# Kernel tuning notes

Hardware: AMD Instinct MI355X
Metric: run time of the kernel (lower is better)

Reference implementation:

```python
import jax, jax.numpy as jnp
import numpy as np

N = 50000
E = 800000
IN_C = 128
HID = 64
HEADS = 4
NEG_SLOPE = 0.2
EPS = 1e-16


def setup_inputs() -> dict:
    key = jax.random.key(0)
    ks = jax.random.split(key, 12)
    x = jax.random.normal(ks[0], (N, IN_C), dtype=jnp.float32)
    edge_index = jax.random.randint(ks[1], (2, E), 0, N, dtype=jnp.int64)
    # layer 1: in -> (HEADS, HID), concat heads
    W1 = jax.random.normal(ks[2], (IN_C, HEADS * HID), dtype=jnp.float32) * (1.0 / np.sqrt(IN_C))
    a_src1 = jax.random.normal(ks[3], (HEADS, HID), dtype=jnp.float32) * 0.1
    a_dst1 = jax.random.normal(ks[4], (HEADS, HID), dtype=jnp.float32) * 0.1
    b1 = jnp.zeros((HEADS * HID,), dtype=jnp.float32)
    # layer 2: HEADS*HID -> (1, HID)
    W2 = jax.random.normal(ks[5], (HEADS * HID, HID), dtype=jnp.float32) * (1.0 / np.sqrt(HEADS * HID))
    a_src2 = jax.random.normal(ks[6], (1, HID), dtype=jnp.float32) * 0.1
    a_dst2 = jax.random.normal(ks[7], (1, HID), dtype=jnp.float32) * 0.1
    b2 = jnp.zeros((HID,), dtype=jnp.float32)
    return {"x": x, "edge_index": edge_index, "W1": W1, "a_src1": a_src1,
            "a_dst1": a_dst1, "b1": b1, "W2": W2, "a_src2": a_src2,
            "a_dst2": a_dst2, "b2": b2}


def _gat_conv(x, src, dst, W, a_src, a_dst, bias, heads, ch):
    n = x.shape[0]
    h = (x @ W).reshape(n, heads, ch)                       # [N,H,C]
    alpha_s = jnp.einsum('nhc,hc->nh', h, a_src)            # [N,H]
    alpha_d = jnp.einsum('nhc,hc->nh', h, a_dst)            # [N,H]
    e = jax.nn.leaky_relu(alpha_s[src] + alpha_d[dst], NEG_SLOPE)  # [E,H]
    # segment softmax over incoming edges of each dst node
    m = jax.ops.segment_max(e, dst, num_segments=n)         # [N,H]
    ex = jnp.exp(e - m[dst])
    denom = jax.ops.segment_sum(ex, dst, num_segments=n)    # [N,H]
    alpha = ex / (denom[dst] + EPS)                         # [E,H]
    msg = h[src] * alpha[:, :, None]                        # [E,H,C]
    out = jax.ops.segment_sum(msg, dst, num_segments=n)     # [N,H,C]
    return out.reshape(n, heads * ch) + bias


def reference(x, edge_index, W1, a_src1, a_dst1, b1, W2, a_src2, a_dst2, b2):
    src = edge_index[0]
    dst = edge_index[1]
    h = _gat_conv(x, src, dst, W1, a_src1, a_dst1, b1, HEADS, HID)
    h = jax.nn.elu(h)
    h = _gat_conv(h, src, dst, W2, a_src2, a_dst2, b2, 1, HID)
    h = jax.nn.elu(h)
    return h  # [N, HID] (output_dim == hidden_channels so no final linear)
```

## Files before the change

### kernel.cpp

```cpp
#include <hip/hip_runtime.h>
#include <math.h>

#define NN 50000
#define EE 800000
#define IN_C 128
#define HID 64
#define HEADS 4
#define EEP 950000
#define SCAN_BLOCKS ((NN + 255) / 256)
#define EBLOCKS ((EE + 255) / 256)

typedef __attribute__((ext_vector_type(8))) short bf16x8;
typedef __attribute__((ext_vector_type(4))) float f32x4;

#if defined(__has_builtin)
#if __has_builtin(__builtin_amdgcn_fdot2_f32_bf16)
#define HAVE_FDOT2_BF16 1
#endif
#endif


__device__ inline unsigned short f2bf(float f) {
    unsigned u = __float_as_uint(f);
    return (unsigned short)((u + 0x7fff + ((u >> 16) & 1)) >> 16);
}
__device__ inline float bf2f(unsigned short s) {
    return __uint_as_float(((unsigned)s) << 16);
}
__device__ inline unsigned prm(unsigned a, unsigned b, unsigned sel) {
    return __builtin_amdgcn_perm(a, b, sel);
}
#ifdef HAVE_FDOT2_BF16
typedef __attribute__((ext_vector_type(2))) __bf16 bf2v;
__device__ inline float fdot2bf(unsigned h, unsigned w, float acc) {
    return __builtin_amdgcn_fdot2_f32_bf16(__builtin_bit_cast(bf2v, h),
                                           __builtin_bit_cast(bf2v, w), acc, false);
}
#else
__device__ inline float fdot2bf(unsigned h, unsigned w, float acc) {
    return acc + bf2f((unsigned short)(h & 0xffff)) * bf2f((unsigned short)(w & 0xffff))
               + bf2f((unsigned short)(h >> 16)) * bf2f((unsigned short)(w >> 16));
}
#endif

__device__ inline int wave_incl_scan(int v, int lane) {
    #pragma unroll
    for (int off = 1; off < 64; off <<= 1) {
        int t = __shfl_up(v, off);
        if (lane >= off) v += t;
    }
    return v;
}

__device__ inline int block256_excl_scan(int v, int tid, int* ws4) {
    int lane = tid & 63, wv = tid >> 6;
    int incl = wave_incl_scan(v, lane);
    if (lane == 63) ws4[wv] = incl;
    __syncthreads();
    if (tid == 0) {
        int run = 0;
        #pragma unroll
        for (int i = 0; i < 4; i++) { int t = ws4[i]; ws4[i] = run; run += t; }
    }
    __syncthreads();
    return incl + ws4[wv] - v;
}


__global__ void front_kernel(const int* __restrict__ ei, int* __restrict__ deg,
                             unsigned short* __restrict__ rank,
                             const float* __restrict__ W1, unsigned short* __restrict__ W1Thi,
                             unsigned short* __restrict__ W1Tlo,
                             const float* __restrict__ W2, unsigned short* __restrict__ W2Thi,
                             unsigned short* __restrict__ W2Tlo) {
    int b = blockIdx.x;
    int tid = threadIdx.x;
    if (b < EBLOCKS) {
        int i = b * 256 + tid;
        if (i < EE) rank[i] = (unsigned short)atomicAdd(&deg[ei[EE + i]], 1);
    } else if (b < EBLOCKS + 128) {
        int idx = (b - EBLOCKS) * 256 + tid;
        int r = idx >> 8, c = idx & 255;
        float v = W1[idx];
        unsigned short h = f2bf(v);
        W1Thi[c * 128 + r] = h;
        W1Tlo[c * 128 + r] = f2bf(v - bf2f(h));
    } else {
        int idx = (b - EBLOCKS - 128) * 256 + tid;
        int r = idx >> 6, c = idx & 63;
        float v = W2[idx];
        unsigned short h = f2bf(v);
        W2Thi[c * 256 + r] = h;
        W2Tlo[c * 256 + r] = f2bf(v - bf2f(h));
    }
}

__global__ void scan_fill_kernel(const int* __restrict__ deg,
                                 unsigned long long* __restrict__ desc,
                                 int* __restrict__ row_ptr,
                                 unsigned short* __restrict__ csr_src) {
    __shared__ int ws4[4];
    __shared__ int sbase;
    int b = blockIdx.x, tid = threadIdx.x;
    int idx = b * 256 + tid;
    int draw = (idx < NN) ? deg[idx] : 0;
    int d = (draw + 3) & ~3;
    int excl = block256_excl_scan(d, tid, ws4);
    if (tid == 255) {
        unsigned total = (unsigned)(excl + d);
        __threadfence();
        atomicExch(&desc[b], (1ULL << 32) | (unsigned long long)total);
    }
    if (tid < 64) {
        int sum = 0;
        int hi = b;
        while (hi > 0) {
            int lo = hi - 64; if (lo < 0) lo = 0;
            int myi = lo + tid;
            unsigned v = 0;
            if (myi < hi) {
                unsigned long long d8;
                do { d8 = atomicAdd(&desc[myi], 0ULL); } while ((d8 >> 32) == 0);
                v = (unsigned)(d8 & 0xffffffffULL);
            }
            #pragma unroll
            for (int off = 32; off; off >>= 1) v += __shfl_down(v, off);
            v = __shfl(v, 0);
            sum += (int)v;
            hi = lo;
        }
        if (tid == 0) sbase = sum;
    }
    __syncthreads();
    int gbase = sbase;
    if (idx < NN) {
        int rp = gbase + excl;
        row_ptr[idx] = rp;
        for (int p = rp + draw; p < rp + d; ++p) csr_src[p] = 0;
    }
    if (b == gridDim.x - 1 && tid == 255) row_ptr[NN] = gbase + excl + d;
}

__global__ void scatter_kernel(const int* __restrict__ ei, const unsigned short* __restrict__ rank,
                               const int* __restrict__ row_ptr, unsigned short* __restrict__ csr_src) {
    int i = blockIdx.x * blockDim.x + threadIdx.x;
    if (i < EE) {
        int d = ei[EE + i];
        csr_src[row_ptr[d] + (int)rank[i]] = (unsigned short)ei[i];
    }
}

__global__ __launch_bounds__(256) void gemm1_mfma(
        const float* __restrict__ x,
        const unsigned short* __restrict__ Bhi, const unsigned short* __restrict__ Blo,
        const float* __restrict__ a_src, const float* __restrict__ a_dst,
        unsigned short* __restrict__ h1b, float* __restrict__ as1, float* __restrict__ ad1) {
    __shared__ unsigned short Ahi[64][136];
    __shared__ unsigned short Alo[64][136];
    int tid = threadIdx.x;
    int w = tid >> 6, lane = tid & 63;
    int lq = lane >> 4, lr = lane & 15;
    int brow = blockIdx.x * 64;
    {
        int row = tid >> 2;
        int col0 = (tid & 3) * 32;
        int gr = min(brow + row, NN - 1);
        #pragma unroll
        for (int i = 0; i < 32; i += 4) {
            float4 v = *(const float4*)(x + (size_t)gr * 128 + col0 + i);
            unsigned short h0 = f2bf(v.x), h1 = f2bf(v.y), h2 = f2bf(v.z), h3 = f2bf(v.w);
            Ahi[row][col0 + i + 0] = h0; Alo[row][col0 + i + 0] = f2bf(v.x - bf2f(h0));
            Ahi[row][col0 + i + 1] = h1; Alo[row][col0 + i + 1] = f2bf(v.y - bf2f(h1));
            Ahi[row][col0 + i + 2] = h2; Alo[row][col0 + i + 2] = f2bf(v.z - bf2f(h2));
            Ahi[row][col0 + i + 3] = h3; Alo[row][col0 + i + 3] = f2bf(v.w - bf2f(h3));
        }
    }
    __syncthreads();
    f32x4 acc[4][4];
    f32x4 zf = {0.f, 0.f, 0.f, 0.f};
    #pragma unroll
    for (int mi = 0; mi < 4; mi++)
        #pragma unroll
        for (int ni = 0; ni < 4; ni++) acc[mi][ni] = zf;
    #pragma unroll
    for (int q = 0; q < 4; q++) {
        int ko = q * 32 + lq * 8;
        bf16x8 ah[4], al[4];
        #pragma unroll
        for (int mi = 0; mi < 4; mi++) {
            ah[mi] = *(const bf16x8*)(const void*)&Ahi[mi * 16 + lr][ko];
            al[mi] = *(const bf16x8*)(const void*)&Alo[mi * 16 + lr][ko];
        }
        #pragma unroll
        for (int ni = 0; ni < 4; ni++) {
            size_t bo = (size_t)(w * 64 + ni * 16 + lr) * 128 + ko;
            bf16x8 bh = *(const bf16x8*)(const void*)(Bhi + bo);
            bf16x8 bl = *(const bf16x8*)(const void*)(Blo + bo);
            #pragma unroll
            for (int mi = 0; mi < 4; mi++) {
                acc[mi][ni] = __builtin_amdgcn_mfma_f32_16x16x32_bf16(al[mi], bh, acc[mi][ni], 0, 0, 0);
                acc[mi][ni] = __builtin_amdgcn_mfma_f32_16x16x32_bf16(ah[mi], bl, acc[mi][ni], 0, 0, 0);
                acc[mi][ni] = __builtin_amdgcn_mfma_f32_16x16x32_bf16(ah[mi], bh, acc[mi][ni], 0, 0, 0);
            }
        }
    }
    float asv[4], adv[4];
    #pragma unroll
    for (int ni = 0; ni < 4; ni++) {
        asv[ni] = a_src[w * 64 + ni * 16 + lr];
        adv[ni] = a_dst[w * 64 + ni * 16 + lr];
    }
    #pragma unroll
    for (int mi = 0; mi < 4; mi++) {
        f32x4 ps = zf, pd = zf;
        #pragma unroll
        for (int ni = 0; ni < 4; ni++)
            #pragma unroll
            for (int r = 0; r < 4; r++) {
                ps[r] += acc[mi][ni][r] * asv[ni];
                pd[r] += acc[mi][ni][r] * adv[ni];
            }
        #pragma unroll
        for (int m = 1; m < 16; m <<= 1)
            #pragma unroll
            for (int r = 0; r < 4; r++) {
                ps[r] += __shfl_xor(ps[r], m);
                pd[r] += __shfl_xor(pd[r], m);
            }
        #pragma unroll
        for (int r = 0; r < 4; r++) {
            int n = brow + mi * 16 + lq * 4 + r;
            if (lr == 0 && n < NN) { as1[n * 4 + w] = ps[r]; ad1[n * 4 + w] = pd[r]; }
        }
        #pragma unroll
        for (int ni = 0; ni < 4; ni++)
            #pragma unroll
            for (int r = 0; r < 4; r++) {
                int n = brow + mi * 16 + lq * 4 + r;
                if (n < NN)
                    h1b[(size_t)n * 256 + w * 64 + ni * 16 + lr] = f2bf(acc[mi][ni][r]);
            }
    }
}

__global__ __launch_bounds__(256) void gemm2_mfma(
        const unsigned short* __restrict__ Ab,
        const unsigned short* __restrict__ Bhi, const unsigned short* __restrict__ Blo,
        const float* __restrict__ a_src, const float* __restrict__ a_dst,
        unsigned short* __restrict__ g2b, float* __restrict__ as2, float* __restrict__ ad2) {
    int tid = threadIdx.x;
    int w = tid >> 6, lane = tid & 63;
    int lq = lane >> 4, lr = lane & 15;
    int wrow = blockIdx.x * 128 + w * 32;
    f32x4 acc[2][4];
    f32x4 zf = {0.f, 0.f, 0.f, 0.f};
    #pragma unroll
    for (int mi = 0; mi < 2; mi++)
        #pragma unroll
        for (int ni = 0; ni < 4; ni++) acc[mi][ni] = zf;
    int ra = min(wrow + lr, NN - 1);
    int rb = min(wrow + 16 + lr, NN - 1);
    #pragma unroll
    for (int q = 0; q < 8; q++) {
        int ko = q * 32 + lq * 8;
        bf16x8 ah0 = *(const bf16x8*)(const void*)(Ab + (size_t)ra * 256 + ko);
        bf16x8 ah1 = *(const bf16x8*)(const void*)(Ab + (size_t)rb * 256 + ko);
        #pragma unroll
        for (int ni = 0; ni < 4; ni++) {
            size_t bo = (size_t)(ni * 16 + lr) * 256 + ko;
            bf16x8 bh = *(const bf16x8*)(const void*)(Bhi + bo);
            bf16x8 bl = *(const bf16x8*)(const void*)(Blo + bo);
            acc[0][ni] = __builtin_amdgcn_mfma_f32_16x16x32_bf16(ah0, bl, acc[0][ni], 0, 0, 0);
            acc[0][ni] = __builtin_amdgcn_mfma_f32_16x16x32_bf16(ah0, bh, acc[0][ni], 0, 0, 0);
            acc[1][ni] = __builtin_amdgcn_mfma_f32_16x16x32_bf16(ah1, bl, acc[1][ni], 0, 0, 0);
            acc[1][ni] = __builtin_amdgcn_mfma_f32_16x16x32_bf16(ah1, bh, acc[1][ni], 0, 0, 0);
        }
    }
    float asv[4], adv[4];
    #pragma unroll
    for (int ni = 0; ni < 4; ni++) {
        asv[ni] = a_src[ni * 16 + lr];
        adv[ni] = a_dst[ni * 16 + lr];
    }
    #pragma unroll
    for (int mi = 0; mi < 2; mi++) {
        f32x4 ps = zf, pd = zf;
        #pragma unroll
        for (int ni = 0; ni < 4; ni++)
            #pragma unroll
            for (int r = 0; r < 4; r++) {
                ps[r] += acc[mi][ni][r] * asv[ni];
                pd[r] += acc[mi][ni][r] * adv[ni];
            }
        #pragma unroll
        for (int m = 1; m < 16; m <<= 1)
            #pragma unroll
            for (int r = 0; r < 4; r++) {
                ps[r] += __shfl_xor(ps[r], m);
                pd[r] += __shfl_xor(pd[r], m);
            }
        #pragma unroll
        for (int r = 0; r < 4; r++) {
            int n = wrow + mi * 16 + lq * 4 + r;
            if (lr == 0 && n < NN) { as2[n] = ps[r]; ad2[n] = pd[r]; }
        }
        #pragma unroll
        for (int ni = 0; ni < 4; ni++)
            #pragma unroll
            for (int r = 0; r < 4; r++) {
                int n = wrow + mi * 16 + lq * 4 + r;
                if (n < NN)
                    g2b[(size_t)n * 64 + ni * 16 + lr] = f2bf(acc[mi][ni][r]);
            }
    }
}

__global__ __launch_bounds__(256, 4) void agg1_kernel(
        const unsigned short* __restrict__ h1b, const int* __restrict__ row_ptr,
        const int* __restrict__ deg, const unsigned short* __restrict__ csr_src,
        const float* __restrict__ as, const float* __restrict__ ad,
        const float* __restrict__ b1, unsigned short* __restrict__ h2b) {
    __shared__ unsigned ssrc32[4][32];
    __shared__ unsigned wpk[4][4][33];
    int tid = threadIdx.x;
    int wv = tid >> 6, lane = tid & 63;
    int n = blockIdx.x * 4 + wv;
    if (n >= NN) return;
    int start = row_ptr[n], end = row_ptr[n + 1];
    int real_end = start + deg[n];
    int H = lane >> 5, l5 = lane & 31;
    int h = l5 >> 3;
    const unsigned short* __restrict__ hp = h1b + l5 * 8;
    float4 adv = ((const float4*)ad)[n];
    f32x4 a0 = {0.f, 0.f, 0.f, 0.f}, a1 = {0.f, 0.f, 0.f, 0.f};
    float d0 = 0.f, d1 = 0.f, d2 = 0.f, d3 = 0.f;
    uint4 LA0, LB0, LA1, LB1;
    unsigned wp0, wp1;
    for (int c0 = start; c0 < end; c0 += 64) {
        int m = min(64, end - c0);
        if (lane < (m >> 1))
            ssrc32[wv][lane] = *(const unsigned*)(const void*)(csr_src + c0 + 2 * lane);
        float x0 = 0.f, x1 = 0.f, x2 = 0.f, x3 = 0.f;
        if (c0 + lane < real_end) {
            int s = (int)csr_src[c0 + lane];
            float4 av = ((const float4*)as)[s];
            float e0 = av.x + adv.x; e0 = e0 > 0.f ? e0 : 0.2f * e0; x0 = __expf(e0);
            float e1 = av.y + adv.y; e1 = e1 > 0.f ? e1 : 0.2f * e1; x1 = __expf(e1);
            float e2 = av.z + adv.z; e2 = e2 > 0.f ? e2 : 0.2f * e2; x2 = __expf(e2);
            float e3 = av.w + adv.w; e3 = e3 > 0.f ? e3 : 0.2f * e3; x3 = __expf(e3);
            d0 += x0; d1 += x1; d2 += x2; d3 += x3;
        }
        unsigned p0 = f2bf(x0), p1 = f2bf(x1), p2 = f2bf(x2), p3 = f2bf(x3);
        unsigned q0 = (unsigned)__shfl_down((int)p0, 1);
        unsigned q1 = (unsigned)__shfl_down((int)p1, 1);
        unsigned q2 = (unsigned)__shfl_down((int)p2, 1);
        unsigned q3 = (unsigned)__shfl_down((int)p3, 1);
        if (((lane & 1) == 0) && lane < m) {
            wpk[wv][0][lane >> 1] = p0 | (q0 << 16);
            wpk[wv][1][lane >> 1] = p1 | (q1 << 16);
            wpk[wv][2][lane >> 1] = p2 | (q2 << 16);
            wpk[wv][3][lane >> 1] = p3 | (q3 << 16);
        }
        int G = m >> 2;
        auto LD = [&](int g, uint4& A, uint4& B, unsigned& wp) {
            unsigned both = ssrc32[wv][2 * g + H];
            int ia = (int)(both & 0xffffu), ib = (int)(both >> 16);
            A = *(const uint4*)(const void*)(hp + ia * 256);
            B = *(const uint4*)(const void*)(hp + ib * 256);
            wp = wpk[wv][h][2 * g + H];
        };
        auto CMP = [&](const uint4& A, const uint4& B, unsigned wp) {
            a0.x = fdot2bf(prm(B.x, A.x, 0x05040100), wp, a0.x);
            a0.y = fdot2bf(prm(B.x, A.x, 0x07060302), wp, a0.y);
            a0.z = fdot2bf(prm(B.y, A.y, 0x05040100), wp, a0.z);
            a0.w = fdot2bf(prm(B.y, A.y, 0x07060302), wp, a0.w);
            a1.x = fdot2bf(prm(B.z, A.z, 0x05040100), wp, a1.x);
            a1.y = fdot2bf(prm(B.z, A.z, 0x07060302), wp, a1.y);
            a1.z = fdot2bf(prm(B.w, A.w, 0x05040100), wp, a1.z);
            a1.w = fdot2bf(prm(B.w, A.w, 0x07060302), wp, a1.w);
        };
        LD(0, LA0, LB0, wp0);
        if (G > 1) LD(1, LA1, LB1, wp1);
        int g = 0;
        while (true) {
            CMP(LA0, LB0, wp0);
            if (g + 2 < G) LD(g + 2, LA0, LB0, wp0);
            if (++g >= G) break;
            CMP(LA1, LB1, wp1);
            if (g + 2 < G) LD(g + 2, LA1, LB1, wp1);
            if (++g >= G) break;
        }
    }
    #pragma unroll
    for (int off = 32; off; off >>= 1) {
        d0 += __shfl_down(d0, off); d1 += __shfl_down(d1, off);
        d2 += __shfl_down(d2, off); d3 += __shfl_down(d3, off);
    }
    d0 = __shfl(d0, 0); d1 = __shfl(d1, 0);
    d2 = __shfl(d2, 0); d3 = __shfl(d3, 0);
    float den = h == 0 ? d0 : h == 1 ? d1 : h == 2 ? d2 : d3;
    a0.x += __shfl_xor(a0.x, 32); a0.y += __shfl_xor(a0.y, 32);
    a0.z += __shfl_xor(a0.z, 32); a0.w += __shfl_xor(a0.w, 32);
    a1.x += __shfl_xor(a1.x, 32); a1.y += __shfl_xor(a1.y, 32);
    a1.z += __shfl_xor(a1.z, 32); a1.w += __shfl_xor(a1.w, 32);
    if (H == 0) {
        float inv = 1.f / (den + 1e-16f);
        float4 bb0 = *(const float4*)(b1 + l5 * 8);
        float4 bb1 = *(const float4*)(b1 + l5 * 8 + 4);
        float r0 = a0.x * inv + bb0.x, r1 = a0.y * inv + bb0.y;
        float r2 = a0.z * inv + bb0.z, r3 = a0.w * inv + bb0.w;
        float r4 = a1.x * inv + bb1.x, r5 = a1.y * inv + bb1.y;
        float r6 = a1.z * inv + bb1.z, r7 = a1.w * inv + bb1.w;
        r0 = r0 > 0.f ? r0 : expm1f(r0); r1 = r1 > 0.f ? r1 : expm1f(r1);
        r2 = r2 > 0.f ? r2 : expm1f(r2); r3 = r3 > 0.f ? r3 : expm1f(r3);
        r4 = r4 > 0.f ? r4 : expm1f(r4); r5 = r5 > 0.f ? r5 : expm1f(r5);
        r6 = r6 > 0.f ? r6 : expm1f(r6); r7 = r7 > 0.f ? r7 : expm1f(r7);
        uint4 st;
        st.x = (unsigned)f2bf(r0) | ((unsigned)f2bf(r1) << 16);
        st.y = (unsigned)f2bf(r2) | ((unsigned)f2bf(r3) << 16);
        st.z = (unsigned)f2bf(r4) | ((unsigned)f2bf(r5) << 16);
        st.w = (unsigned)f2bf(r6) | ((unsigned)f2bf(r7) << 16);
        *(uint4*)(void*)(h2b + (size_t)n * 256 + l5 * 8) = st;
    }
}

__global__ __launch_bounds__(256, 4) void agg2_kernel(
        const unsigned short* __restrict__ g2b, const int* __restrict__ row_ptr,
        const int* __restrict__ deg, const unsigned short* __restrict__ csr_src,
        const float* __restrict__ as, const float* __restrict__ ad,
        const float* __restrict__ b2, float* __restrict__ out) {
    __shared__ unsigned ssrc32[4][32];
    __shared__ unsigned wpk2[4][32];
    int tid = threadIdx.x;
    int wv = tid >> 6, lane = tid & 63;
    int n = blockIdx.x * 4 + wv;
    if (n >= NN) return;
    int start = row_ptr[n], end = row_ptr[n + 1];
    int real_end = start + deg[n];
    int H = lane >> 5, l5 = lane & 31;
    const unsigned short* __restrict__ gp = g2b + l5 * 2;
    float adv = ad[n];
    float ax = 0.f, ay = 0.f;
    float dsum = 0.f;
    unsigned A0, B0, w0, A1, B1, w1v;
    for (int c0 = start; c0 < end; c0 += 64) {
        int m = min(64, end - c0);
        if (lane < (m >> 1))
            ssrc32[wv][lane] = *(const unsigned*)(const void*)(csr_src + c0 + 2 * lane);
        float x = 0.f;
        if (c0 + lane < real_end) {
            int s = (int)csr_src[c0 + lane];
            float e = as[s] + adv;
            e = e > 0.f ? e : 0.2f * e;
            x = __expf(e);
            dsum += x;
        }
        unsigned p = f2bf(x);
        unsigned q = (unsigned)__shfl_down((int)p, 1);
        if (((lane & 1) == 0) && lane < m) wpk2[wv][lane >> 1] = p | (q << 16);
        int G = m >> 2;
        auto LD = [&](int g, unsigned& A, unsigned& B, unsigned& wp) {
            unsigned both = ssrc32[wv][2 * g + H];
            int ia = (int)(both & 0xffffu), ib = (int)(both >> 16);
            A = *(const unsigned*)(const void*)(gp + ia * 64);
            B = *(const unsigned*)(const void*)(gp + ib * 64);
            wp = wpk2[wv][2 * g + H];
        };
        auto CMP = [&](unsigned A, unsigned B, unsigned wp) {
            ax = fdot2bf(prm(B, A, 0x05040100), wp, ax);
            ay = fdot2bf(prm(B, A, 0x07060302), wp, ay);
        };
        LD(0, A0, B0, w0);
        if (G > 1) LD(1, A1, B1, w1v);
        int g = 0;
        while (true) {
            CMP(A0, B0, w0);
            if (g + 2 < G) LD(g + 2, A0, B0, w0);
            if (++g >= G) break;
            CMP(A1, B1, w1v);
            if (g + 2 < G) LD(g + 2, A1, B1, w1v);
            if (++g >= G) break;
        }
    }
    #pragma unroll
    for (int off = 32; off; off >>= 1) dsum += __shfl_down(dsum, off);
    dsum = __shfl(dsum, 0);
    ax += __shfl_xor(ax, 32);
    ay += __shfl_xor(ay, 32);
    if (H == 0) {
        float inv = 1.f / (dsum + 1e-16f);
        float2 bv = ((const float2*)b2)[l5];
        float rx = ax * inv + bv.x;
        float ry = ay * inv + bv.y;
        rx = rx > 0.f ? rx : expm1f(rx);
        ry = ry > 0.f ? ry : expm1f(ry);
        *(float2*)(out + (size_t)n * 64 + l5 * 2) = make_float2(rx, ry);
    }
}


extern "C" void kernel_launch(void* const* d_in, const int* in_sizes, int n_in,
                              void* d_out, int out_size, void* d_ws, size_t ws_size,
                              hipStream_t stream) {
    const float* x      = (const float*)d_in[0];
    const int*   ei     = (const int*)d_in[1];
    const float* W1     = (const float*)d_in[2];
    const float* a_src1 = (const float*)d_in[3];
    const float* a_dst1 = (const float*)d_in[4];
    const float* b1     = (const float*)d_in[5];
    const float* W2     = (const float*)d_in[6];
    const float* a_src2 = (const float*)d_in[7];
    const float* a_dst2 = (const float*)d_in[8];
    const float* b2     = (const float*)d_in[9];
    float* out = (float*)d_out;

    char* base = (char*)d_ws;
    size_t off = 0;
    auto alloc = [&](size_t bytes) -> void* {
        void* p = base + off;
        off = (off + bytes + 255) & ~(size_t)255;
        return p;
    };
    int*   deg     = (int*)alloc(NN * sizeof(int));
    unsigned long long* desc = (unsigned long long*)alloc(SCAN_BLOCKS * sizeof(unsigned long long));
    unsigned short* rank = (unsigned short*)alloc(EE * sizeof(unsigned short));
    int*   row_ptr = (int*)alloc((NN + 1) * sizeof(int));
    unsigned short* csr_src = (unsigned short*)alloc((size_t)EEP * sizeof(unsigned short));
    unsigned short* W1Thi = (unsigned short*)alloc(256 * 128 * 2);
    unsigned short* W1Tlo = (unsigned short*)alloc(256 * 128 * 2);
    unsigned short* W2Thi = (unsigned short*)alloc(64 * 256 * 2);
    unsigned short* W2Tlo = (unsigned short*)alloc(64 * 256 * 2);
    unsigned short* h1b   = (unsigned short*)alloc((size_t)NN * 256 * 2);
    float* as1     = (float*)alloc((size_t)NN * 4 * sizeof(float));
    float* ad1     = (float*)alloc((size_t)NN * 4 * sizeof(float));
    unsigned short* h2b   = (unsigned short*)alloc((size_t)NN * 256 * 2);
    unsigned short* g2b = h1b;
    float* as2 = as1;
    float* ad2 = ad1;

    size_t clear_bytes = (size_t)((char*)(desc + SCAN_BLOCKS) - (char*)deg);
    hipMemsetAsync(deg, 0, clear_bytes, stream);

    front_kernel<<<EBLOCKS + 128 + 64, 256, 0, stream>>>(ei, deg, rank, W1, W1Thi, W1Tlo,
                                                         W2, W2Thi, W2Tlo);
    scan_fill_kernel<<<SCAN_BLOCKS, 256, 0, stream>>>(deg, desc, row_ptr, csr_src);
    scatter_kernel<<<EBLOCKS, 256, 0, stream>>>(ei, rank, row_ptr, csr_src);

    gemm1_mfma<<<(NN + 63) / 64, 256, 0, stream>>>(x, W1Thi, W1Tlo,
                                                   a_src1, a_dst1, h1b, as1, ad1);
    agg1_kernel<<<(NN + 3) / 4, 256, 0, stream>>>(h1b, row_ptr, deg, csr_src,
                                                  as1, ad1, b1, h2b);
    gemm2_mfma<<<(NN + 127) / 128, 256, 0, stream>>>(h2b, W2Thi, W2Tlo,
                                                     a_src2, a_dst2, g2b, as2, ad2);
    agg2_kernel<<<(NN + 3) / 4, 256, 0, stream>>>(g2b, row_ptr, deg, csr_src,
                                                  as2, ad2, b2, out);
}
```

Measured before the change: 290.8 us.

## Remap layer-1 softmax weights to one lane per edge-head and read src from LDS

In agg1, the per-edge attention weights are now computed with lanes split as 4 heads × 16 edges. Each lane handles one head for a subset of edges, which replaces the single-lane computation of all four heads. The source index is now read from the shared-memory copy instead of reloaded from global memory, in both aggregation kernels. Also swaps expm1f for __expf-1 in ELU and rewrites leaky ReLU with fmax/fmin, trading a little accuracy near zero for cheaper math.

```diff
diff --git a/kernel.cpp b/kernel.cpp
--- a/kernel.cpp
+++ b/kernel.cpp
@@ -330,36 +330,32 @@
     int real_end = start + deg[n];
     int H = lane >> 5, l5 = lane & 31;
     int h = l5 >> 3;
+    int hW = lane >> 4;
+    int eSub = lane & 15;
     const unsigned short* __restrict__ hp = h1b + l5 * 8;
-    float4 adv = ((const float4*)ad)[n];
+    float adW = ad[(size_t)n * 4 + hW];
     f32x4 a0 = {0.f, 0.f, 0.f, 0.f}, a1 = {0.f, 0.f, 0.f, 0.f};
-    float d0 = 0.f, d1 = 0.f, d2 = 0.f, d3 = 0.f;
+    float dsum = 0.f;
     uint4 LA0, LB0, LA1, LB1;
     unsigned wp0, wp1;
     for (int c0 = start; c0 < end; c0 += 64) {
         int m = min(64, end - c0);
         if (lane < (m >> 1))
             ssrc32[wv][lane] = *(const unsigned*)(const void*)(csr_src + c0 + 2 * lane);
-        float x0 = 0.f, x1 = 0.f, x2 = 0.f, x3 = 0.f;
-        if (c0 + lane < real_end) {
-            int s = (int)csr_src[c0 + lane];
-            float4 av = ((const float4*)as)[s];
-            float e0 = av.x + adv.x; e0 = e0 > 0.f ? e0 : 0.2f * e0; x0 = __expf(e0);
-            float e1 = av.y + adv.y; e1 = e1 > 0.f ? e1 : 0.2f * e1; x1 = __expf(e1);
-            float e2 = av.z + adv.z; e2 = e2 > 0.f ? e2 : 0.2f * e2; x2 = __expf(e2);
-            float e3 = av.w + adv.w; e3 = e3 > 0.f ? e3 : 0.2f * e3; x3 = __expf(e3);
-            d0 += x0; d1 += x1; d2 += x2; d3 += x3;
-        }
-        unsigned p0 = f2bf(x0), p1 = f2bf(x1), p2 = f2bf(x2), p3 = f2bf(x3);
-        unsigned q0 = (unsigned)__shfl_down((int)p0, 1);
-        unsigned q1 = (unsigned)__shfl_down((int)p1, 1);
-        unsigned q2 = (unsigned)__shfl_down((int)p2, 1);
-        unsigned q3 = (unsigned)__shfl_down((int)p3, 1);
-        if (((lane & 1) == 0) && lane < m) {
-            wpk[wv][0][lane >> 1] = p0 | (q0 << 16);
-            wpk[wv][1][lane >> 1] = p1 | (q1 << 16);
-            wpk[wv][2][lane >> 1] = p2 | (q2 << 16);
-            wpk[wv][3][lane >> 1] = p3 | (q3 << 16);
+        for (int eb = 0; eb < m; eb += 16) {
+            int j = eb + eSub;
+            unsigned pairw = ssrc32[wv][j >> 1];
+            float x = 0.f;
+            if (c0 + j < real_end) {
+                int s = (int)((pairw >> ((j & 1) << 4)) & 0xffffu);
+                float e = as[(size_t)s * 4 + hW] + adW;
+                e = fmaxf(e, 0.f) + 0.2f * fminf(e, 0.f);
+                x = __expf(e);
+                dsum += x;
+            }
+            unsigned p = f2bf(x);
+            unsigned q = (unsigned)__shfl_down((int)p, 1);
+            if ((eSub & 1) == 0 && j < m) wpk[wv][hW][j >> 1] = p | (q << 16);
         }
         int G = m >> 2;
         auto LD = [&](int g, uint4& A, uint4& B, unsigned& wp) {
@@ -392,13 +388,8 @@
         }
     }
     #pragma unroll
-    for (int off = 32; off; off >>= 1) {
-        d0 += __shfl_down(d0, off); d1 += __shfl_down(d1, off);
-        d2 += __shfl_down(d2, off); d3 += __shfl_down(d3, off);
-    }
-    d0 = __shfl(d0, 0); d1 = __shfl(d1, 0);
-    d2 = __shfl(d2, 0); d3 = __shfl(d3, 0);
-    float den = h == 0 ? d0 : h == 1 ? d1 : h == 2 ? d2 : d3;
+    for (int off = 1; off < 16; off <<= 1) dsum += __shfl_xor(dsum, off);
+    float den = __shfl(dsum, ((lane & 31) >> 3) << 4);
     a0.x += __shfl_xor(a0.x, 32); a0.y += __shfl_xor(a0.y, 32);
     a0.z += __shfl_xor(a0.z, 32); a0.w += __shfl_xor(a0.w, 32);
     a1.x += __shfl_xor(a1.x, 32); a1.y += __shfl_xor(a1.y, 32);
@@ -411,10 +402,10 @@
         float r2 = a0.z * inv + bb0.z, r3 = a0.w * inv + bb0.w;
         float r4 = a1.x * inv + bb1.x, r5 = a1.y * inv + bb1.y;
         float r6 = a1.z * inv + bb1.z, r7 = a1.w * inv + bb1.w;
-        r0 = r0 > 0.f ? r0 : expm1f(r0); r1 = r1 > 0.f ? r1 : expm1f(r1);
-        r2 = r2 > 0.f ? r2 : expm1f(r2); r3 = r3 > 0.f ? r3 : expm1f(r3);
-        r4 = r4 > 0.f ? r4 : expm1f(r4); r5 = r5 > 0.f ? r5 : expm1f(r5);
-        r6 = r6 > 0.f ? r6 : expm1f(r6); r7 = r7 > 0.f ? r7 : expm1f(r7);
+        r0 = r0 > 0.f ? r0 : __expf(r0) - 1.f; r1 = r1 > 0.f ? r1 : __expf(r1) - 1.f;
+        r2 = r2 > 0.f ? r2 : __expf(r2) - 1.f; r3 = r3 > 0.f ? r3 : __expf(r3) - 1.f;
+        r4 = r4 > 0.f ? r4 : __expf(r4) - 1.f; r5 = r5 > 0.f ? r5 : __expf(r5) - 1.f;
+        r6 = r6 > 0.f ? r6 : __expf(r6) - 1.f; r7 = r7 > 0.f ? r7 : __expf(r7) - 1.f;
         uint4 st;
         st.x = (unsigned)f2bf(r0) | ((unsigned)f2bf(r1) << 16);
         st.y = (unsigned)f2bf(r2) | ((unsigned)f2bf(r3) << 16);
@@ -449,9 +440,10 @@
             ssrc32[wv][lane] = *(const unsigned*)(const void*)(csr_src + c0 + 2 * lane);
         float x = 0.f;
         if (c0 + lane < real_end) {
-            int s = (int)csr_src[c0 + lane];
+            unsigned pw = ssrc32[wv][lane >> 1];
+            int s = (int)((pw >> ((lane & 1) << 4)) & 0xffffu);
             float e = as[s] + adv;
-            e = e > 0.f ? e : 0.2f * e;
+            e = fmaxf(e, 0.f) + 0.2f * fminf(e, 0.f);
             x = __expf(e);
             dsum += x;
         }
@@ -492,8 +484,8 @@
         float2 bv = ((const float2*)b2)[l5];
         float rx = ax * inv + bv.x;
         float ry = ay * inv + bv.y;
-        rx = rx > 0.f ? rx : expm1f(rx);
-        ry = ry > 0.f ? ry : expm1f(ry);
+        rx = rx > 0.f ? rx : __expf(rx) - 1.f;
+        ry = ry > 0.f ? ry : __expf(ry) - 1.f;
         *(float2*)(out + (size_t)n * 64 + l5 * 2) = make_float2(rx, ry);
     }
 }
```

Result: no change. 285.2 us (-1.9%).
